# Kernel tuning notes

Measured on AMD Instinct MI355X. Metric: run time of the kernel, lower is better.

The kernel has to match this reference:

```python
import jax, jax.numpy as jnp
import numpy as np

N_NODES = 50000
N_EDGES = 800000
IN_FEAT = 128
HID = 128
OUT = 10
N_GRAPHS = 128
BN_EPS = 1e-5


def setup_inputs() -> dict:
    key = jax.random.key(0)
    ks = jax.random.split(key, 16)
    inp = {
        "n_feat": jax.random.normal(ks[0], (N_NODES, IN_FEAT), dtype=jnp.float32),
        "src": jax.random.randint(ks[1], (N_EDGES,), 0, N_NODES),
        "dst": jax.random.randint(ks[2], (N_EDGES,), 0, N_NODES),
        "graph_ids": jnp.sort(jax.random.randint(ks[3], (N_NODES,), 0, N_GRAPHS)),
        # GraphConv weights (DGL layout: weight [in, out], bias [out])
        "W1": jax.random.normal(ks[4], (IN_FEAT, HID), dtype=jnp.float32) / np.sqrt(IN_FEAT),
        "b1": jnp.zeros((HID,), dtype=jnp.float32),
        "W2": jax.random.normal(ks[5], (HID, HID), dtype=jnp.float32) / np.sqrt(HID),
        "b2": jnp.zeros((HID,), dtype=jnp.float32),
        # BatchNorm1d affine params
        "gamma": jnp.ones((HID,), dtype=jnp.float32),
        "beta": jnp.zeros((HID,), dtype=jnp.float32),
        # MLP head
        "fc1_w": jax.random.normal(ks[6], (HID, HID), dtype=jnp.float32) / np.sqrt(HID),
        "fc1_b": jnp.zeros((HID,), dtype=jnp.float32),
        "fc2_w": jax.random.normal(ks[7], (HID, OUT), dtype=jnp.float32) / np.sqrt(HID),
        "fc2_b": jnp.zeros((OUT,), dtype=jnp.float32),
    }
    return inp


def _graph_conv(x, W, b, src, dst, inv_sqrt_out, inv_sqrt_in):
    # DGL GraphConv, norm='both': h = D_in^{-1/2} A D_out^{-1/2} x W + b
    h = x * inv_sqrt_out[:, None]          # [N, d_in]
    h = h @ W                              # [N, d_out] (project before gather: fewer bytes moved)
    agg = jax.ops.segment_sum(h[src], dst, num_segments=N_NODES)  # gather + scatter-add
    return agg * inv_sqrt_in[:, None] + b


def reference(n_feat, src, dst, graph_ids, W1, b1, W2, b2, gamma, beta,
              fc1_w, fc1_b, fc2_w, fc2_b):
    ones_e = jnp.ones((N_EDGES,), dtype=jnp.float32)
    deg_out = jnp.clip(jax.ops.segment_sum(ones_e, src, num_segments=N_NODES), 1.0)
    deg_in = jnp.clip(jax.ops.segment_sum(ones_e, dst, num_segments=N_NODES), 1.0)
    inv_sqrt_out = jax.lax.rsqrt(deg_out)
    inv_sqrt_in = jax.lax.rsqrt(deg_in)

    x = jax.nn.relu(_graph_conv(n_feat, W1, b1, src, dst, inv_sqrt_out, inv_sqrt_in))
    # dropout is identity in eval mode
    x = jax.nn.relu(_graph_conv(x, W2, b2, src, dst, inv_sqrt_out, inv_sqrt_in))

    # SumPooling over graphs
    embedding = jax.ops.segment_sum(x, graph_ids, num_segments=N_GRAPHS)  # [B, HID]

    # BatchNorm1d (training-mode batch stats, biased variance like torch)
    mu = jnp.mean(embedding, axis=0)
    var = jnp.mean(jnp.square(embedding - mu), axis=0)
    h = gamma * (embedding - mu) * jax.lax.rsqrt(var + BN_EPS) + beta

    h = jax.nn.relu(h @ fc1_w + fc1_b)
    logits = h @ fc2_w + fc2_b
    return embedding, jax.nn.log_softmax(logits, axis=-1)
```

## Files before the change

kernel.cpp:

```cpp
#include <hip/hip_runtime.h>
#include <hip/hip_bf16.h>
#include <math.h>

#define N_NODES 50000
#define N_EDGES 800000
#define HID 128
#define N_GRAPHS 128
#define OUTC 10
#define BN_EPS 1e-5f

#define SCAN_B 256
#define N_SCAN_BLOCKS ((N_NODES + SCAN_B - 1) / SCAN_B)

#define POOL_CHUNK 32
#define N_POOL_BLOCKS ((N_NODES + POOL_CHUNK - 1) / POOL_CHUNK)

#define HB 128
#define HW8 (N_NODES / 4)
#define HR_B 256
#define HR_BLOCKS ((HW8 + HR_B - 1) / HR_B)

#define EPAD 8
#define E_SRC_CAP (N_EDGES + N_NODES * EPAD)

#define LDA 136

#define MM_BLOCKS ((N_NODES + 64) / 64)

#define AGG_NODES 16
#define AGG_BLOCKS (N_NODES / AGG_NODES)

typedef short short8 __attribute__((ext_vector_type(8)));
typedef float floatx4 __attribute__((ext_vector_type(4)));

template <typename T, typename F>
__device__ inline T bitcast(F f) {
    union { F a; T b; } u;
    u.a = f;
    return u.b;
}

__device__ inline unsigned short f2bf(float x) {
    return __hip_bfloat16_raw(__float2bfloat16(x)).x;
}

__global__ __launch_bounds__(1024) void hist_part_kernel(const int* __restrict__ src,
                                                         const int* __restrict__ dst,
                                                         unsigned int* __restrict__ part,
                                                         const float* __restrict__ W1,
                                                         const float* __restrict__ W2,
                                                         unsigned short* __restrict__ Wp) {
    if (blockIdx.x == 2 * HB) {
        for (int q = threadIdx.x; q < 4096; q += 1024) {
            int wi = q >> 11;
            const float* __restrict__ W = wi ? W2 : W1;
            int t2 = q & 2047;
            int tile = t2 >> 6, lane = t2 & 63;
            int kc = tile >> 3, nt = tile & 7;
            int n = lane & 15, quad = lane >> 4;
            unsigned short v[8];
#pragma unroll
            for (int j = 0; j < 8; j++) {
                int k = kc * 32 + quad * 8 + j;
                v[j] = f2bf(W[k * HID + nt * 16 + n]);
            }
            *(uint4*)&Wp[(size_t)q * 8] = *(uint4*)v;
        }
        return;
    }
    __shared__ unsigned int h[HW8];
    for (int i = threadIdx.x; i < HW8; i += 1024) h[i] = 0;
    __syncthreads();
    int half = (blockIdx.x >= HB) ? 1 : 0;
    const int* __restrict__ idx = half ? dst : src;
    int b = blockIdx.x - half * HB;
    for (int e = b * 1024 + threadIdx.x; e < N_EDGES; e += HB * 1024) {
        int v = idx[e];
        atomicAdd(&h[v >> 2], 1u << ((v & 3) << 3));
    }
    __syncthreads();
    unsigned int* __restrict__ out = part + (size_t)blockIdx.x * HW8;
    for (int i = threadIdx.x; i < HW8; i += 1024) out[i] = h[i];
}

__global__ __launch_bounds__(HR_B) void hist_reduce_kernel(unsigned int* __restrict__ part,
                                                           int* __restrict__ cnt_in,
                                                           float* __restrict__ inv_out,
                                                           float* __restrict__ inv_in,
                                                           int* __restrict__ bsum) {
    int t = threadIdx.x;
    int w = blockIdx.x * HR_B + t;
    int padsum = 0;
    if (w < HW8) {
        unsigned int s = 0, d = 0;
        for (int b = 0; b < HB; b++) {
            s += part[(size_t)b * HW8 + w];
            unsigned int c = part[(size_t)(b + HB) * HW8 + w];
            part[(size_t)(b + HB) * HW8 + w] = d;
            d += c;
        }
#pragma unroll
        for (int j = 0; j < 4; j++) {
            int i = w * 4 + j;
            int so = (int)((s >> (j * 8)) & 0xFFu);
            int di = (int)((d >> (j * 8)) & 0xFFu);
            cnt_in[i] = di;
            inv_out[i] = rsqrtf(fmaxf((float)so, 1.0f));
            inv_in[i] = rsqrtf(fmaxf((float)di, 1.0f));
            padsum += (di + EPAD - 1) & ~(EPAD - 1);
        }
    }
#pragma unroll
    for (int o = 32; o > 0; o >>= 1) padsum += __shfl_xor(padsum, o);
    if ((t & 63) == 0) bsum[blockIdx.x * 4 + (t >> 6)] = padsum;
}

__device__ inline void mm_tail(const unsigned short* __restrict__ xs,
                               const unsigned short* __restrict__ Wp,
                               __hip_bfloat16* __restrict__ Y, int row0) {
    int tid = threadIdx.x;
    int wave = tid >> 6, lane = tid & 63;
    int m = lane & 15, quad = lane >> 4;
    int rowl = wave * 16;

    short8 a[4];
#pragma unroll
    for (int kc = 0; kc < 4; kc++)
        a[kc] = bitcast<short8>(*(const uint4*)&xs[(rowl + m) * LDA + kc * 32 + quad * 8]);

    floatx4 acc[8];
#pragma unroll
    for (int nt = 0; nt < 8; nt++) acc[nt] = (floatx4){0.f, 0.f, 0.f, 0.f};

#pragma unroll
    for (int nt = 0; nt < 8; nt++) {
#pragma unroll
        for (int kc = 0; kc < 4; kc++) {
            short8 bfr = bitcast<short8>(
                *(const uint4*)&Wp[((size_t)(kc * 8 + nt) * 64 + lane) * 8]);
            acc[nt] = __builtin_amdgcn_mfma_f32_16x16x32_bf16(a[kc], bfr, acc[nt], 0, 0, 0);
        }
    }

#pragma unroll
    for (int nt = 0; nt < 8; nt++) {
#pragma unroll
        for (int i = 0; i < 4; i++) {
            int rg = row0 + rowl + quad * 4 + i;
            if (rg < N_NODES + 1) {
                Y[(size_t)rg * HID + nt * 16 + m] = __float2bfloat16(acc[nt][i]);
            }
        }
    }
}

__global__ __launch_bounds__(256) void scanmm1_kernel(const int* __restrict__ cnt,
                                                      const int* __restrict__ bsum,
                                                      int* __restrict__ row_ptr,
                                                      int* __restrict__ edge_src,
                                                      const float* __restrict__ X,
                                                      const float* __restrict__ scale,
                                                      const unsigned short* __restrict__ Wp,
                                                      __hip_bfloat16* __restrict__ Y,
                                                      float* __restrict__ emb) {
    __shared__ unsigned short xs[64 * LDA];
    int t = threadIdx.x;
    int b = blockIdx.x;

    if (b >= N_SCAN_BLOCKS) {
        if (b == N_SCAN_BLOCKS + MM_BLOCKS) {
            for (int i = t; i < N_GRAPHS * HID; i += 256) emb[i] = 0.f;
            return;
        }
        int row0 = (b - N_SCAN_BLOCKS) * 64;
        for (int j = 0; j < 8; j++) {
            int idx4 = j * 256 + t;
            int r = idx4 >> 5;
            int col = (idx4 & 31) * 4;
            int rg = row0 + r;
            float4 v = make_float4(0.f, 0.f, 0.f, 0.f);
            if (rg < N_NODES) {
                v = *(const float4*)&X[(size_t)rg * HID + col];
                float sc = scale[rg];
                v.x *= sc; v.y *= sc; v.z *= sc; v.w *= sc;
            }
            unsigned short o[4];
            o[0] = f2bf(v.x); o[1] = f2bf(v.y); o[2] = f2bf(v.z); o[3] = f2bf(v.w);
            *(ushort4*)&xs[r * LDA + col] = *(ushort4*)o;
        }
        __syncthreads();
        mm_tail(xs, Wp, Y, row0);
        return;
    }

    int* sb = (int*)xs;
    int* part = (int*)xs + 256;
    sb[t] = (t < N_SCAN_BLOCKS) ? bsum[t] : 0;
    __syncthreads();
    for (int off = 1; off < SCAN_B; off <<= 1) {
        int u = (t >= off) ? sb[t - off] : 0;
        __syncthreads();
        sb[t] += u;
        __syncthreads();
    }
    int boff = (b == 0) ? 0 : sb[b - 1];

    int i = b * SCAN_B + t;
    int raw = (i < N_NODES) ? cnt[i] : 0;
    int v = (raw + EPAD - 1) & ~(EPAD - 1);
    part[t] = v;
    __syncthreads();
    for (int off = 1; off < SCAN_B; off <<= 1) {
        int u = (t >= off) ? part[t - off] : 0;
        __syncthreads();
        part[t] += u;
        __syncthreads();
    }
    if (i < N_NODES) {
        int ex = part[t] - v + boff;
        row_ptr[i] = ex;
        for (int p = ex + raw; p < ex + v; p++) edge_src[p] = N_NODES;
        if (i == N_NODES - 1) row_ptr[N_NODES] = ex + v;
    }
}

__global__ __launch_bounds__(1024) void csr_fill_kernel(const int* __restrict__ src,
                                                        const int* __restrict__ dst,
                                                        const unsigned int* __restrict__ part,
                                                        const int* __restrict__ row_ptr,
                                                        int* __restrict__ edge_src) {
    __shared__ unsigned int loc[HW8];
    int b = blockIdx.x;
    const unsigned int* __restrict__ off = part + (size_t)(b + HB) * HW8;
    for (int i = threadIdx.x; i < HW8; i += 1024) loc[i] = off[i];
    __syncthreads();
    for (int e = b * 1024 + threadIdx.x; e < N_EDGES; e += HB * 1024) {
        int d = dst[e];
        unsigned int old = atomicAdd(&loc[d >> 2], 1u << ((d & 3) << 3));
        int local = (int)((old >> ((d & 3) << 3)) & 0xFFu);
        edge_src[row_ptr[d] + local] = src[e];
    }
}

#define ACC8(u)                                                                              \
    acc[0] += __uint_as_float(u.x << 16); acc[1] += __uint_as_float(u.x & 0xFFFF0000u);      \
    acc[2] += __uint_as_float(u.y << 16); acc[3] += __uint_as_float(u.y & 0xFFFF0000u);      \
    acc[4] += __uint_as_float(u.z << 16); acc[5] += __uint_as_float(u.z & 0xFFFF0000u);      \
    acc[6] += __uint_as_float(u.w << 16); acc[7] += __uint_as_float(u.w & 0xFFFF0000u);

#define GATHER_BODY(idxv)                                                                    \
    {                                                                                        \
        int j = 0;                                                                           \
        for (; j + 16 <= mm; j += 16) {                                                      \
            int s0 = __shfl(idxv, j + esub);                                                 \
            int s1 = __shfl(idxv, j + 4 + esub);                                             \
            int s2 = __shfl(idxv, j + 8 + esub);                                             \
            int s3 = __shfl(idxv, j + 12 + esub);                                            \
            uint4 u0 = Yq[s0 * (HID / 8) + f16];                                             \
            uint4 u1 = Yq[s1 * (HID / 8) + f16];                                             \
            uint4 u2 = Yq[s2 * (HID / 8) + f16];                                             \
            uint4 u3 = Yq[s3 * (HID / 8) + f16];                                             \
            ACC8(u0); ACC8(u1); ACC8(u2); ACC8(u3);                                          \
        }                                                                                    \
        if (j < mm) {                                                                        \
            int s0 = __shfl(idxv, j + esub);                                                 \
            int s1 = __shfl(idxv, j + 4 + esub);                                             \
            uint4 u0 = Yq[s0 * (HID / 8) + f16];                                             \
            uint4 u1 = Yq[s1 * (HID / 8) + f16];                                             \
            ACC8(u0); ACC8(u1);                                                              \
        }                                                                                    \
    }

__global__ __launch_bounds__(256) void agg1mm2_kernel(const __hip_bfloat16* __restrict__ Y1,
                                                      const int* __restrict__ edge_src,
                                                      const int* __restrict__ row_ptr,
                                                      const float* __restrict__ inv_in,
                                                      const float* __restrict__ inv_out,
                                                      const float* __restrict__ bias,
                                                      const unsigned short* __restrict__ Wp2,
                                                      __hip_bfloat16* __restrict__ Y2) {
    if (blockIdx.x == AGG_BLOCKS) {
        if (threadIdx.x < 16) {
            uint4 z = make_uint4(0u, 0u, 0u, 0u);
            *(uint4*)&Y2[(size_t)N_NODES * HID + threadIdx.x * 8] = z;
        }
        return;
    }
    __shared__ unsigned short xs[AGG_NODES * LDA];
    const uint4* __restrict__ Yq = (const uint4*)Y1;
    int wave = threadIdx.x >> 6;
    int lane = threadIdx.x & 63;
    int esub = lane >> 4;
    int f16 = lane & 15;
    int nb = blockIdx.x * AGG_NODES + wave * 4;

    int begs[4], ends[4], idx0[4];
#pragma unroll
    for (int it = 0; it < 4; it++) {
        begs[it] = row_ptr[nb + it];
        ends[it] = row_ptr[nb + it + 1];
    }
#pragma unroll
    for (int it = 0; it < 4; it++) {
        int mm0 = min(64, ends[it] - begs[it]);
        idx0[it] = (lane < mm0) ? edge_src[begs[it] + lane] : N_NODES;
    }

    for (int it = 0; it < 4; it++) {
        int n = nb + it;
        int beg = begs[it], end = ends[it];
        float acc[8] = {};
        int idx = idx0[it];
        for (int base = beg; base < end; base += 64) {
            int mm = min(64, end - base);
            if (base > beg) idx = (lane < mm) ? edge_src[base + lane] : N_NODES;
            GATHER_BODY(idx);
        }
#pragma unroll
        for (int i = 0; i < 8; i++) {
            acc[i] += __shfl_xor(acc[i], 16);
            acc[i] += __shfl_xor(acc[i], 32);
        }
        if (lane < 16) {
            float si = inv_in[n];
            float so = inv_out[n];
            int f0 = f16 * 8;
            float4 b0 = *(const float4*)&bias[f0];
            float4 b1 = *(const float4*)&bias[f0 + 4];
            unsigned short u[8];
            u[0] = f2bf(fmaxf(acc[0] * si + b0.x, 0.f) * so);
            u[1] = f2bf(fmaxf(acc[1] * si + b0.y, 0.f) * so);
            u[2] = f2bf(fmaxf(acc[2] * si + b0.z, 0.f) * so);
            u[3] = f2bf(fmaxf(acc[3] * si + b0.w, 0.f) * so);
            u[4] = f2bf(fmaxf(acc[4] * si + b1.x, 0.f) * so);
            u[5] = f2bf(fmaxf(acc[5] * si + b1.y, 0.f) * so);
            u[6] = f2bf(fmaxf(acc[6] * si + b1.z, 0.f) * so);
            u[7] = f2bf(fmaxf(acc[7] * si + b1.w, 0.f) * so);
            *(uint4*)&xs[(wave * 4 + it) * LDA + f0] = *(uint4*)u;
        }
    }
    __syncthreads();

    int m = lane & 15, quad = lane >> 4;
    short8 a[4];
#pragma unroll
    for (int kc = 0; kc < 4; kc++)
        a[kc] = bitcast<short8>(*(const uint4*)&xs[m * LDA + kc * 32 + quad * 8]);
#pragma unroll
    for (int w2 = 0; w2 < 2; w2++) {
        int nt = wave * 2 + w2;
        floatx4 acc2 = (floatx4){0.f, 0.f, 0.f, 0.f};
#pragma unroll
        for (int kc = 0; kc < 4; kc++) {
            short8 bfr = bitcast<short8>(
                *(const uint4*)&Wp2[((size_t)(kc * 8 + nt) * 64 + lane) * 8]);
            acc2 = __builtin_amdgcn_mfma_f32_16x16x32_bf16(a[kc], bfr, acc2, 0, 0, 0);
        }
#pragma unroll
        for (int i = 0; i < 4; i++) {
            int rg = blockIdx.x * AGG_NODES + quad * 4 + i;
            Y2[(size_t)rg * HID + nt * 16 + m] = __float2bfloat16(acc2[i]);
        }
    }
}

__global__ __launch_bounds__(256) void agg2_kernel(const __hip_bfloat16* __restrict__ Y,
                                                   const int* __restrict__ edge_src,
                                                   const int* __restrict__ row_ptr,
                                                   const float* __restrict__ inv_in,
                                                   const float* __restrict__ bias,
                                                   float* __restrict__ Xout) {
    const uint4* __restrict__ Yq = (const uint4*)Y;
    int wave = threadIdx.x >> 6;
    int lane = threadIdx.x & 63;
    int esub = lane >> 4;
    int f16 = lane & 15;
    int nb = blockIdx.x * AGG_NODES + wave * 4;

    int begs[4], ends[4], idx0[4];
#pragma unroll
    for (int it = 0; it < 4; it++) {
        begs[it] = row_ptr[nb + it];
        ends[it] = row_ptr[nb + it + 1];
    }
#pragma unroll
    for (int it = 0; it < 4; it++) {
        int mm0 = min(64, ends[it] - begs[it]);
        idx0[it] = (lane < mm0) ? edge_src[begs[it] + lane] : N_NODES;
    }

    for (int it = 0; it < 4; it++) {
        int n = nb + it;
        int beg = begs[it], end = ends[it];
        float acc[8] = {};
        int idx = idx0[it];
        for (int base = beg; base < end; base += 64) {
            int mm = min(64, end - base);
            if (base > beg) idx = (lane < mm) ? edge_src[base + lane] : N_NODES;
            GATHER_BODY(idx);
        }
#pragma unroll
        for (int i = 0; i < 8; i++) {
            acc[i] += __shfl_xor(acc[i], 16);
            acc[i] += __shfl_xor(acc[i], 32);
        }
        if (lane < 16) {
            float si = inv_in[n];
            int f0 = f16 * 8;
            float4 b0 = *(const float4*)&bias[f0];
            float4 b1 = *(const float4*)&bias[f0 + 4];
            float4 o0, o1;
            o0.x = fmaxf(acc[0] * si + b0.x, 0.f);
            o0.y = fmaxf(acc[1] * si + b0.y, 0.f);
            o0.z = fmaxf(acc[2] * si + b0.z, 0.f);
            o0.w = fmaxf(acc[3] * si + b0.w, 0.f);
            o1.x = fmaxf(acc[4] * si + b1.x, 0.f);
            o1.y = fmaxf(acc[5] * si + b1.y, 0.f);
            o1.z = fmaxf(acc[6] * si + b1.z, 0.f);
            o1.w = fmaxf(acc[7] * si + b1.w, 0.f);
            *(float4*)&Xout[(size_t)n * HID + f0] = o0;
            *(float4*)&Xout[(size_t)n * HID + f0 + 4] = o1;
        }
    }
}

__global__ __launch_bounds__(64) void pool_kernel(const float* __restrict__ X,
                                                  const int* __restrict__ gid,
                                                  float* __restrict__ emb) {
    int lane = threadIdx.x;
    int n0 = blockIdx.x * POOL_CHUNK;
    int n1 = min(n0 + POOL_CHUNK, N_NODES);
    if (n0 >= N_NODES) return;
    int g_cur = gid[n0];
    float ax = 0.f, ay = 0.f;
    for (int n = n0; n < n1; n++) {
        int g = gid[n];
        if (g != g_cur) {
            atomicAdd(&emb[g_cur * HID + lane * 2], ax);
            atomicAdd(&emb[g_cur * HID + lane * 2 + 1], ay);
            ax = 0.f; ay = 0.f;
            g_cur = g;
        }
        float2 v = *(const float2*)&X[(size_t)n * HID + lane * 2];
        ax += v.x;
        ay += v.y;
    }
    atomicAdd(&emb[g_cur * HID + lane * 2], ax);
    atomicAdd(&emb[g_cur * HID + lane * 2 + 1], ay);
}

__global__ __launch_bounds__(128) void head_fused_kernel(const float* __restrict__ emb,
                                                         const float* __restrict__ gamma,
                                                         const float* __restrict__ beta,
                                                         const float* __restrict__ fc1_w,
                                                         const float* __restrict__ fc1_b,
                                                         const float* __restrict__ fc2_w,
                                                         const float* __restrict__ fc2_b,
                                                         float* __restrict__ out) {
    int r = blockIdx.x, f = threadIdx.x;
    float s = 0.f;
    for (int row = 0; row < N_GRAPHS; row++) s += emb[row * HID + f];
    float mu = s * (1.f / N_GRAPHS);
    float v = 0.f;
    for (int row = 0; row < N_GRAPHS; row++) {
        float d = emb[row * HID + f] - mu;
        v += d * d;
    }
    v *= (1.f / N_GRAPHS);
    float sc = gamma[f] * rsqrtf(v + BN_EPS);
    float sh = beta[f] - mu * sc;

    __shared__ float xr[HID];
    xr[f] = emb[r * HID + f] * sc + sh;
    __syncthreads();
    float acc = fc1_b[f];
    for (int k = 0; k < HID; k++) acc += xr[k] * fc1_w[k * HID + f];
    __shared__ float hr[HID];
    hr[f] = fmaxf(acc, 0.f);
    __syncthreads();

    __shared__ float logits[OUTC];
    __shared__ float mstat[2];
    if (f < OUTC) {
        float a = fc2_b[f];
        for (int k = 0; k < HID; k++) a += hr[k] * fc2_w[k * OUTC + f];
        logits[f] = a;
    }
    __syncthreads();
    if (f == 0) {
        float m = logits[0];
        for (int o = 1; o < OUTC; o++) m = fmaxf(m, logits[o]);
        float sum = 0.f;
        for (int o = 0; o < OUTC; o++) sum += expf(logits[o] - m);
        mstat[0] = m;
        mstat[1] = logf(sum);
    }
    __syncthreads();
    if (f < OUTC) out[r * OUTC + f] = logits[f] - mstat[0] - mstat[1];
}

extern "C" void kernel_launch(void* const* d_in, const int* in_sizes, int n_in,
                              void* d_out, int out_size, void* d_ws, size_t ws_size,
                              hipStream_t stream) {
    const float* n_feat = (const float*)d_in[0];
    const int*   src    = (const int*)d_in[1];
    const int*   dst    = (const int*)d_in[2];
    const int*   gid    = (const int*)d_in[3];
    const float* W1     = (const float*)d_in[4];
    const float* b1     = (const float*)d_in[5];
    const float* W2     = (const float*)d_in[6];
    const float* b2     = (const float*)d_in[7];
    const float* gamma  = (const float*)d_in[8];
    const float* beta   = (const float*)d_in[9];
    const float* fc1_w  = (const float*)d_in[10];
    const float* fc1_b  = (const float*)d_in[11];
    const float* fc2_w  = (const float*)d_in[12];
    const float* fc2_b  = (const float*)d_in[13];

    char* wsb = (char*)d_ws;
    size_t off = 0;
    auto alloc = [&](size_t bytes) -> void* {
        void* p = wsb + off;
        off += (bytes + 255) & ~(size_t)255;
        return p;
    };
    int*   cnt_in  = (int*)alloc((size_t)N_NODES * 4);
    int*   row_ptr = (int*)alloc((size_t)(N_NODES + 1) * 4);
    int*   e_src   = (int*)alloc((size_t)E_SRC_CAP * 4);
    float* inv_out = (float*)alloc((size_t)N_NODES * 4);
    float* inv_in  = (float*)alloc((size_t)N_NODES * 4);
    unsigned int* part = (unsigned int*)alloc((size_t)2 * HB * HW8 * 4);
    __hip_bfloat16* Y1 = (__hip_bfloat16*)alloc((size_t)(N_NODES + 1) * HID * 2);
    __hip_bfloat16* Y2 = (__hip_bfloat16*)alloc((size_t)(N_NODES + 1) * HID * 2);
    float* X       = (float*)alloc((size_t)N_NODES * HID * 4);
    unsigned short* Wp = (unsigned short*)alloc((size_t)2 * 32 * 64 * 8 * 2);
    int*   bsum    = (int*)alloc((size_t)SCAN_B * 4);

    float* emb_out = (float*)d_out;
    float* lsm_out = emb_out + N_GRAPHS * HID;

    hist_part_kernel<<<2 * HB + 1, 1024, 0, stream>>>(src, dst, part, W1, W2, Wp);
    hist_reduce_kernel<<<HR_BLOCKS, HR_B, 0, stream>>>(part, cnt_in, inv_out, inv_in, bsum);
    scanmm1_kernel<<<N_SCAN_BLOCKS + MM_BLOCKS + 1, 256, 0, stream>>>(
        cnt_in, bsum, row_ptr, e_src, n_feat, inv_out, Wp, Y1, emb_out);
    csr_fill_kernel<<<HB, 1024, 0, stream>>>(src, dst, part, row_ptr, e_src);

    agg1mm2_kernel<<<AGG_BLOCKS + 1, 256, 0, stream>>>(Y1, e_src, row_ptr, inv_in, inv_out,
                                                       b1, Wp + (size_t)32 * 64 * 8, Y2);
    agg2_kernel<<<AGG_BLOCKS, 256, 0, stream>>>(Y2, e_src, row_ptr, inv_in, b2, X);

    pool_kernel<<<N_POOL_BLOCKS, 64, 0, stream>>>(X, gid, emb_out);
    head_fused_kernel<<<N_GRAPHS, HID, 0, stream>>>(emb_out, gamma, beta, fc1_w, fc1_b,
                                                    fc2_w, fc2_b, lsm_out);
}
```

Measured before the change: 235.0 us.

## Fuse second aggregation with sum pooling via per-block partial slots

```diff
diff --git a/kernel.cpp b/kernel.cpp
--- a/kernel.cpp
+++ b/kernel.cpp
@@ -12,9 +12,6 @@
 #define SCAN_B 256
 #define N_SCAN_BLOCKS ((N_NODES + SCAN_B - 1) / SCAN_B)
 
-#define POOL_CHUNK 32
-#define N_POOL_BLOCKS ((N_NODES + POOL_CHUNK - 1) / POOL_CHUNK)
-
 #define HB 128
 #define HW8 (N_NODES / 4)
 #define HR_B 256
@@ -24,11 +21,14 @@
 #define E_SRC_CAP (N_EDGES + N_NODES * EPAD)
 
 #define LDA 136
+#define LDAF 132
 
 #define MM_BLOCKS ((N_NODES + 64) / 64)
 
 #define AGG_NODES 16
 #define AGG_BLOCKS (N_NODES / AGG_NODES)
+
+#define PSLOTS 3
 
 typedef short short8 __attribute__((ext_vector_type(8)));
 typedef float floatx4 __attribute__((ext_vector_type(4)));
@@ -162,6 +162,7 @@
                                                       const float* __restrict__ scale,
                                                       const unsigned short* __restrict__ Wp,
                                                       __hip_bfloat16* __restrict__ Y,
+                                                      __hip_bfloat16* __restrict__ Y2,
                                                       float* __restrict__ emb) {
     __shared__ unsigned short xs[64 * LDA];
     int t = threadIdx.x;
@@ -170,6 +171,10 @@
     if (b >= N_SCAN_BLOCKS) {
         if (b == N_SCAN_BLOCKS + MM_BLOCKS) {
             for (int i = t; i < N_GRAPHS * HID; i += 256) emb[i] = 0.f;
+            if (t < 16) {
+                uint4 z = make_uint4(0u, 0u, 0u, 0u);
+                *(uint4*)&Y2[(size_t)N_NODES * HID + t * 8] = z;
+            }
             return;
         }
         int row0 = (b - N_SCAN_BLOCKS) * 64;
@@ -279,13 +284,6 @@
                                                       const float* __restrict__ bias,
                                                       const unsigned short* __restrict__ Wp2,
                                                       __hip_bfloat16* __restrict__ Y2) {
-    if (blockIdx.x == AGG_BLOCKS) {
-        if (threadIdx.x < 16) {
-            uint4 z = make_uint4(0u, 0u, 0u, 0u);
-            *(uint4*)&Y2[(size_t)N_NODES * HID + threadIdx.x * 8] = z;
-        }
-        return;
-    }
     __shared__ unsigned short xs[AGG_NODES * LDA];
     const uint4* __restrict__ Yq = (const uint4*)Y1;
     int wave = threadIdx.x >> 6;
@@ -364,18 +362,27 @@
     }
 }
 
-__global__ __launch_bounds__(256) void agg2_kernel(const __hip_bfloat16* __restrict__ Y,
-                                                   const int* __restrict__ edge_src,
-                                                   const int* __restrict__ row_ptr,
-                                                   const float* __restrict__ inv_in,
-                                                   const float* __restrict__ bias,
-                                                   float* __restrict__ Xout) {
+__global__ __launch_bounds__(256) void agg2pool_kernel(const __hip_bfloat16* __restrict__ Y,
+                                                       const int* __restrict__ edge_src,
+                                                       const int* __restrict__ row_ptr,
+                                                       const float* __restrict__ inv_in,
+                                                       const float* __restrict__ bias,
+                                                       const int* __restrict__ gid,
+                                                       float* __restrict__ pe,
+                                                       int* __restrict__ ptag,
+                                                       float* __restrict__ emb) {
+    __shared__ float xp[AGG_NODES * LDAF];
+    __shared__ int gl[AGG_NODES];
     const uint4* __restrict__ Yq = (const uint4*)Y;
-    int wave = threadIdx.x >> 6;
-    int lane = threadIdx.x & 63;
+    int t = threadIdx.x;
+    int wave = t >> 6;
+    int lane = t & 63;
     int esub = lane >> 4;
     int f16 = lane & 15;
-    int nb = blockIdx.x * AGG_NODES + wave * 4;
+    int nb0 = blockIdx.x * AGG_NODES;
+    int nb = nb0 + wave * 4;
+
+    if (t < AGG_NODES) gl[t] = gid[nb0 + t];
 
     int begs[4], ends[4], idx0[4];
 #pragma unroll
@@ -418,35 +425,73 @@
             o1.y = fmaxf(acc[5] * si + b1.y, 0.f);
             o1.z = fmaxf(acc[6] * si + b1.z, 0.f);
             o1.w = fmaxf(acc[7] * si + b1.w, 0.f);
-            *(float4*)&Xout[(size_t)n * HID + f0] = o0;
-            *(float4*)&Xout[(size_t)n * HID + f0 + 4] = o1;
-        }
-    }
-}
-
-__global__ __launch_bounds__(64) void pool_kernel(const float* __restrict__ X,
-                                                  const int* __restrict__ gid,
-                                                  float* __restrict__ emb) {
-    int lane = threadIdx.x;
-    int n0 = blockIdx.x * POOL_CHUNK;
-    int n1 = min(n0 + POOL_CHUNK, N_NODES);
-    if (n0 >= N_NODES) return;
-    int g_cur = gid[n0];
-    float ax = 0.f, ay = 0.f;
-    for (int n = n0; n < n1; n++) {
-        int g = gid[n];
-        if (g != g_cur) {
-            atomicAdd(&emb[g_cur * HID + lane * 2], ax);
-            atomicAdd(&emb[g_cur * HID + lane * 2 + 1], ay);
-            ax = 0.f; ay = 0.f;
-            g_cur = g;
-        }
-        float2 v = *(const float2*)&X[(size_t)n * HID + lane * 2];
-        ax += v.x;
-        ay += v.y;
-    }
-    atomicAdd(&emb[g_cur * HID + lane * 2], ax);
-    atomicAdd(&emb[g_cur * HID + lane * 2 + 1], ay);
+            *(float4*)&xp[(wave * 4 + it) * LDAF + f0] = o0;
+            *(float4*)&xp[(wave * 4 + it) * LDAF + f0 + 4] = o1;
+        }
+    }
+    __syncthreads();
+
+    if (t < HID) {
+        int f = t;
+        int r = 0;
+        int g = gl[0];
+        float run = 0.f;
+#pragma unroll
+        for (int k = 0; k < AGG_NODES; k++) {
+            int gk = gl[k];
+            if (gk != g) {
+                if (r < PSLOTS) {
+                    pe[((size_t)blockIdx.x * PSLOTS + r) * HID + f] = run;
+                    if (f == 0) ptag[blockIdx.x * PSLOTS + r] = g;
+                } else {
+                    atomicAdd(&emb[g * HID + f], run);
+                }
+                r++;
+                g = gk;
+                run = 0.f;
+            }
+            run += xp[k * LDAF + f];
+        }
+        if (r < PSLOTS) {
+            pe[((size_t)blockIdx.x * PSLOTS + r) * HID + f] = run;
+            if (f == 0) ptag[blockIdx.x * PSLOTS + r] = g;
+        } else {
+            atomicAdd(&emb[g * HID + f], run);
+        }
+        r++;
+        if (f == 0) {
+            for (; r < PSLOTS; r++) ptag[blockIdx.x * PSLOTS + r] = -1;
+        }
+    }
+}
+
+__global__ __launch_bounds__(HID) void pool_reduce_kernel(const float* __restrict__ pe,
+                                                          const int* __restrict__ ptag,
+                                                          const int* __restrict__ gid,
+                                                          float* __restrict__ emb) {
+    int g = blockIdx.x, f = threadIdx.x;
+    __shared__ int bounds[2];
+    if (f == 0) {
+        int lo = 0, hi = N_NODES;
+        while (lo < hi) { int mid = (lo + hi) >> 1; if (gid[mid] < g) lo = mid + 1; else hi = mid; }
+        bounds[0] = lo;
+        hi = N_NODES;
+        while (lo < hi) { int mid = (lo + hi) >> 1; if (gid[mid] <= g) lo = mid + 1; else hi = mid; }
+        bounds[1] = lo;
+    }
+    __syncthreads();
+    int n0 = bounds[0], n1 = bounds[1];
+    float acc = emb[g * HID + f];
+    if (n0 < n1) {
+        int b0 = n0 >> 4, b1 = (n1 - 1) >> 4;
+        for (int b = b0; b <= b1; b++) {
+#pragma unroll
+            for (int r = 0; r < PSLOTS; r++) {
+                if (ptag[b * PSLOTS + r] == g) acc += pe[((size_t)b * PSLOTS + r) * HID + f];
+            }
+        }
+    }
+    emb[g * HID + f] = acc;
 }
 
 __global__ __launch_bounds__(128) void head_fused_kernel(const float* __restrict__ emb,
@@ -532,7 +577,8 @@
     unsigned int* part = (unsigned int*)alloc((size_t)2 * HB * HW8 * 4);
     __hip_bfloat16* Y1 = (__hip_bfloat16*)alloc((size_t)(N_NODES + 1) * HID * 2);
     __hip_bfloat16* Y2 = (__hip_bfloat16*)alloc((size_t)(N_NODES + 1) * HID * 2);
-    float* X       = (float*)alloc((size_t)N_NODES * HID * 4);
+    float* pe      = (float*)alloc((size_t)AGG_BLOCKS * PSLOTS * HID * 4);
+    int*   ptag    = (int*)alloc((size_t)AGG_BLOCKS * PSLOTS * 4);
     unsigned short* Wp = (unsigned short*)alloc((size_t)2 * 32 * 64 * 8 * 2);
     int*   bsum    = (int*)alloc((size_t)SCAN_B * 4);
 
@@ -542,14 +588,14 @@
     hist_part_kernel<<<2 * HB + 1, 1024, 0, stream>>>(src, dst, part, W1, W2, Wp);
     hist_reduce_kernel<<<HR_BLOCKS, HR_B, 0, stream>>>(part, cnt_in, inv_out, inv_in, bsum);
     scanmm1_kernel<<<N_SCAN_BLOCKS + MM_BLOCKS + 1, 256, 0, stream>>>(
-        cnt_in, bsum, row_ptr, e_src, n_feat, inv_out, Wp, Y1, emb_out);
+        cnt_in, bsum, row_ptr, e_src, n_feat, inv_out, Wp, Y1, Y2, emb_out);
     csr_fill_kernel<<<HB, 1024, 0, stream>>>(src, dst, part, row_ptr, e_src);
 
-    agg1mm2_kernel<<<AGG_BLOCKS + 1, 256, 0, stream>>>(Y1, e_src, row_ptr, inv_in, inv_out,
-                                                       b1, Wp + (size_t)32 * 64 * 8, Y2);
-    agg2_kernel<<<AGG_BLOCKS, 256, 0, stream>>>(Y2, e_src, row_ptr, inv_in, b2, X);
-
-    pool_kernel<<<N_POOL_BLOCKS, 64, 0, stream>>>(X, gid, emb_out);
+    agg1mm2_kernel<<<AGG_BLOCKS, 256, 0, stream>>>(Y1, e_src, row_ptr, inv_in, inv_out,
+                                                   b1, Wp + (size_t)32 * 64 * 8, Y2);
+    agg2pool_kernel<<<AGG_BLOCKS, 256, 0, stream>>>(Y2, e_src, row_ptr, inv_in, b2, gid,
+                                                    pe, ptag, emb_out);
+    pool_reduce_kernel<<<N_GRAPHS, HID, 0, stream>>>(pe, ptag, gid, emb_out);
     head_fused_kernel<<<N_GRAPHS, HID, 0, stream>>>(emb_out, gamma, beta, fc1_w, fc1_b,
                                                     fc2_w, fc2_b, lsm_out);
 }
```

Measured after the change: 241.1 us. +2.6%, slower.
